# Optimization experiments

Measured on AMD Instinct MI355X. Metric: run time of the kernel, lower is better.

The kernel has to match this reference:

```python
import jax, jax.numpy as jnp
import numpy as np

B, N, D, A = 2048, 32, 64, 8
MAX_ACTION = 1.0
VARIANCE = 1.0


def setup_inputs() -> dict:
    key = jax.random.key(0)
    k1, k2, k3, k4, k5 = jax.random.split(key, 5)
    mean = jax.random.normal(k1, (B, D), dtype=jnp.float32)
    # SPD covariance: small-scale L L^T + 0.1 I
    L = jax.random.normal(k2, (B, D, D), dtype=jnp.float32) * 0.05
    covariance = jnp.einsum('bij,bkj->bik', L, L) + 0.1 * jnp.eye(D, dtype=jnp.float32)
    centers = jax.random.normal(k3, (N, D), dtype=jnp.float32) * 0.5
    weights = jax.random.normal(k4, (N, A), dtype=jnp.float32) * 0.1
    lengthscales = jnp.ones((D,), dtype=jnp.float32) + 0.1 * jax.random.uniform(k5, (D,), dtype=jnp.float32)
    return {"mean": mean, "covariance": covariance, "centers": centers,
            "weights": weights, "lengthscales": lengthscales}


def squash_sin(mean, covariance, max_action):
    # mean: (B, K); covariance: (B, K, K)
    K = mean.shape[-1]
    ma = jnp.full((K,), max_action, dtype=mean.dtype)
    diag_cov = jnp.diagonal(covariance, axis1=-2, axis2=-1)          # (B, K)
    squashed_mean = ma * jnp.exp(-diag_cov / 2.0) * jnp.sin(mean)
    lq = -(diag_cov[..., :, None] + diag_cov[..., None, :]) / 2.0
    q = jnp.exp(lq)
    mean_diff = mean[..., :, None] - mean[..., None, :]
    mean_sum = mean[..., :, None] + mean[..., None, :]
    sq_cov = ((jnp.exp(lq + covariance) - q) * jnp.cos(mean_diff)
              - (jnp.exp(lq - covariance) - q) * jnp.cos(mean_sum))
    outer_max = ma[None, :] * ma[:, None]
    sq_cov = outer_max * sq_cov / 2.0
    # diag_embed of (B, K) -> (B, K, K)
    cross = (ma * jnp.exp(-diag_cov / 2.0) * jnp.cos(mean))[..., :, None] * jnp.eye(K, dtype=mean.dtype)
    return squashed_mean, sq_cov, cross


def reference(mean, covariance, centers, weights, lengthscales):
    b = mean.shape[0]
    inv_l = 1.0 / lengthscales                                        # (D,)
    # B_mat = diag(inv_l) @ cov @ diag(inv_l) + I  (B, D, D)
    B_mat = covariance * (inv_l[:, None] * inv_l[None, :]) + jnp.eye(D, dtype=mean.dtype)
    inp = centers[None, :, :] - mean[:, None, :]                      # (B, N, D)
    scaled_inp = inp * inv_l                                          # (B, N, D)
    t = jnp.swapaxes(jnp.linalg.solve(B_mat, jnp.swapaxes(scaled_inp, -1, -2)), -1, -2)  # (B, N, D)
    exp_term = jnp.exp(-0.5 * jnp.sum(scaled_inp * t, axis=-1))       # (B, N)
    _, log_det = jnp.linalg.slogdet(B_mat)                            # (B,)
    normalizer = VARIANCE * jnp.exp(-0.5 * log_det)
    phi_mean = normalizer[:, None] * exp_term                         # (B, N)
    action_mean = phi_mean @ weights                                  # (B, A)

    t_scaled = t * inv_l                                              # (B, N, D)
    cross_cov = jnp.einsum('bnd,bna->bda', t_scaled, phi_mean[..., None] * weights)  # (B, D, A)

    diff = centers[:, None, :] - centers[None, :, :]                  # (N, N, D)
    center_bar = (centers[:, None, :] + centers[None, :, :]) / 2.0    # (N, N, D)
    inv_lambda = 1.0 / lengthscales ** 2
    exp1 = -0.25 * jnp.sum(diff ** 2 * inv_lambda, axis=-1)           # (N, N)
    B_q = covariance + jnp.diag(lengthscales ** 2 / 2.0)[None]        # (B, D, D)
    z = center_bar[None] - mean[:, None, None, :]                     # (B, N, N, D)
    z_flat = z.reshape(b, N * N, D)
    solved = jnp.swapaxes(jnp.linalg.solve(B_q, jnp.swapaxes(z_flat, -1, -2)), -1, -2)
    exp2 = (-0.5 * jnp.sum(z_flat * solved, axis=-1)).reshape(b, N, N)
    log_det_lh = jnp.sum(jnp.log(lengthscales ** 2 / 2.0))
    _, log_det_bq = jnp.linalg.slogdet(B_q)
    c_q = jnp.exp(0.5 * (log_det_lh - log_det_bq))                    # (B,)
    Q = (VARIANCE ** 2) * c_q[:, None, None] * jnp.exp(exp1[None] + exp2)  # (B, N, N)

    action_cov = jnp.einsum('na,bnm,mc->bac', weights, Q, weights)    # (B, A, A)
    action_cov = action_cov - action_mean[:, :, None] * action_mean[:, None, :]
    action_cov = (action_cov + jnp.swapaxes(action_cov, -1, -2)) / 2.0
    action_cov = action_cov + jnp.eye(A, dtype=mean.dtype) * 1e-6

    action_mean, action_cov, C = squash_sin(action_mean, action_cov, MAX_ACTION)
    cross_cov = jnp.einsum('bda,bac->bdc', cross_cov, C)
    return (action_mean, action_cov, cross_cov)
```

## Files before the change

kernel.cpp:

```cpp
#include <hip/hip_runtime.h>
#include <math.h>


#define DD 64
#define NN 32
#define AA 8
#define NBATCH 2048
#define STR 68
#define W9 9

__global__ void rbf_prep(const float* __restrict__ centers,
                         const float* __restrict__ ls,
                         float* __restrict__ ws) {
    __shared__ float cen_s[NN * DD];
    __shared__ float il2_s[DD];
    int t = threadIdx.x;
    for (int e = t; e < NN * DD; e += 256) cen_s[e] = centers[e];
    if (t < DD) { float l = ls[t]; il2_s[t] = 1.0f / (l * l); }
    __syncthreads();
    int p = blockIdx.x * 256 + t;
    if (p < NN * NN) {
        int n = p >> 5, m = p & 31;
        float acc = 0.f;
        for (int d = 0; d < DD; ++d) {
            float df = cen_s[n * DD + d] - cen_s[m * DD + d];
            acc += df * df * il2_s[d];
        }
        ws[p] = -0.25f * acc;
    }
    if (blockIdx.x == 0 && t < DD) {
        float l = ls[t];
        float v = logf(0.5f * l * l);
        #pragma unroll
        for (int o = 1; o < 64; o <<= 1) v += __shfl_xor(v, o, 64);
        if (t == 0) ws[NN * NN] = v;
    }
}

__device__ __forceinline__ void factor_panel(float (&A)[4][4], const int p,
    float* __restrict__ LmT, float* __restrict__ diag_s, float* __restrict__ invd_s,
    const int lw)
{
    const int rb  = lw & 15;
    const int cbl = lw >> 4;
    const int c0  = 16 * p + 4 * cbl;
    const int r0  = 4 * rb;
    #pragma unroll
    for (int jj = 0; jj < 16; ++jj) {
        const int q  = jj >> 2;
        const int ci = jj & 3;
        const int j  = 16 * p + jj;
        const int fsrc = rb | (q << 4);
        const int hsrc = (4 * p + cbl) | (q << 4);
        const int dsrc = (4 * p + q) | (q << 4);
        float d  = __shfl(A[ci][ci], dsrc, 64);
        float f0 = __shfl(A[0][ci], fsrc, 64);
        float f1 = __shfl(A[1][ci], fsrc, 64);
        float f2 = __shfl(A[2][ci], fsrc, 64);
        float f3 = __shfl(A[3][ci], fsrc, 64);
        float h0 = __shfl(A[0][ci], hsrc, 64);
        float h1 = __shfl(A[1][ci], hsrc, 64);
        float h2 = __shfl(A[2][ci], hsrc, 64);
        float h3 = __shfl(A[3][ci], hsrc, 64);
        float id = __builtin_amdgcn_rcpf(d);
        float fr[4];
        fr[0] = (r0 + 0 > j) ? f0 : 0.f;
        fr[1] = (r0 + 1 > j) ? f1 : 0.f;
        fr[2] = (r0 + 2 > j) ? f2 : 0.f;
        fr[3] = (r0 + 3 > j) ? f3 : 0.f;
        float hc[4];
        hc[0] = (c0 + 0 > j) ? h0 * id : 0.f;
        hc[1] = (c0 + 1 > j) ? h1 * id : 0.f;
        hc[2] = (c0 + 2 > j) ? h2 * id : 0.f;
        hc[3] = (c0 + 3 > j) ? h3 * id : 0.f;
        #pragma unroll
        for (int s = 0; s < 4; ++s)
            #pragma unroll
            for (int c = 0; c < 4; ++c)
                A[s][c] -= fr[s] * hc[c];
        if (cbl == 0) {
            float4 v = make_float4(fr[0] * id, fr[1] * id, fr[2] * id, fr[3] * id);
            *(float4*)&LmT[j * STR + r0] = v;
        }
        if (lw == jj) { diag_s[j] = d; invd_s[j] = id; }
    }
}

__device__ __forceinline__ void trailing_update2(
    float (&A1)[4][4], float (&A2)[4][4], const int p,
    const float* __restrict__ LmT1, const float* __restrict__ LmT2,
    const float* __restrict__ diag1, const float* __restrict__ diag2,
    const int rb, const int cb, const int cb1)
{
    #pragma unroll 2
    for (int kk = 0; kk < 16; ++kk) {
        const int k = 16 * p + kk;
        const float4 Lr1 = *(const float4*)&LmT1[k * STR + 4 * rb];
        const float4 Lc1 = *(const float4*)&LmT1[k * STR + 4 * cb1];
        const float4 Lr2 = *(const float4*)&LmT2[k * STR + 4 * rb];
        const float4 Lc2 = *(const float4*)&LmT2[k * STR + 4 * cb];
        const float d1 = diag1[k], d2 = diag2[k];
        {
            const float h0 = Lc1.x * d1, h1 = Lc1.y * d1, h2 = Lc1.z * d1, h3 = Lc1.w * d1;
            A1[0][0] -= Lr1.x * h0; A1[0][1] -= Lr1.x * h1; A1[0][2] -= Lr1.x * h2; A1[0][3] -= Lr1.x * h3;
            A1[1][0] -= Lr1.y * h0; A1[1][1] -= Lr1.y * h1; A1[1][2] -= Lr1.y * h2; A1[1][3] -= Lr1.y * h3;
            A1[2][0] -= Lr1.z * h0; A1[2][1] -= Lr1.z * h1; A1[2][2] -= Lr1.z * h2; A1[2][3] -= Lr1.z * h3;
            A1[3][0] -= Lr1.w * h0; A1[3][1] -= Lr1.w * h1; A1[3][2] -= Lr1.w * h2; A1[3][3] -= Lr1.w * h3;
        }
        {
            const float h0 = Lc2.x * d2, h1 = Lc2.y * d2, h2 = Lc2.z * d2, h3 = Lc2.w * d2;
            A2[0][0] -= Lr2.x * h0; A2[0][1] -= Lr2.x * h1; A2[0][2] -= Lr2.x * h2; A2[0][3] -= Lr2.x * h3;
            A2[1][0] -= Lr2.y * h0; A2[1][1] -= Lr2.y * h1; A2[1][2] -= Lr2.y * h2; A2[1][3] -= Lr2.y * h3;
            A2[2][0] -= Lr2.z * h0; A2[2][1] -= Lr2.z * h1; A2[2][2] -= Lr2.z * h2; A2[2][3] -= Lr2.z * h3;
            A2[3][0] -= Lr2.w * h0; A2[3][1] -= Lr2.w * h1; A2[3][2] -= Lr2.w * h2; A2[3][3] -= Lr2.w * h3;
        }
    }
}

__global__ __launch_bounds__(256, 3) void rbf_main(
    const float* __restrict__ mean,
    const float* __restrict__ cov,
    const float* __restrict__ centers,
    const float* __restrict__ weights,
    const float* __restrict__ ls,
    const float* __restrict__ ws,
    float* __restrict__ out)
{
    __shared__ __align__(16) float LmT1[DD * STR];
    __shared__ __align__(16) float LmT2[DD * STR];
    __shared__ __align__(16) float H_s[NN * STR];
    __shared__ __align__(16) float K_s[DD * W9];
    __shared__ __align__(16) float cp_s[DD * W9];
    __shared__ float diag1[DD], invd1[DD], diag2[DD], invd2[DD];
    __shared__ float mean_s[DD], invl_s[DD], l2h_s[DD];
    __shared__ float w9_s[NN * W9], phiw_s[NN * W9], U_s[NN * W9];
    __shared__ float am_s[AA], acr_s[AA * W9], Ca_s[AA];
    __shared__ float ldlh_s;

    const int t   = threadIdx.x;
    const int b   = blockIdx.x;
    const int lw  = t & 63;
    const int wv  = t >> 6;
    const int rb  = t & 15;
    const int cb  = t >> 4;
    const int cb1 = (cb + 8) & 15;
    const int grp = t >> 3;
    const int l8  = t & 7;
    const float* cvb = cov + (size_t)b * DD * DD;

    if (t < DD) {
        float l = ls[t];
        invl_s[t] = 1.0f / l;
        l2h_s[t]  = 0.5f * l * l;
        mean_s[t] = mean[(size_t)b * DD + t];
    }
    w9_s[(t >> 3) * W9 + (t & 7)] = weights[t];
    if (t == 0) ldlh_s = ws[NN * NN];
    __syncthreads();

    float A1[4][4], A2[4][4];
    {
        #pragma unroll
        for (int c = 0; c < 4; ++c) {
            const int gr = 4 * cb + c;
            const float4 cv = *(const float4*)(cvb + (size_t)gr * DD + 4 * rb);
            A2[0][c] = cv.x + ((4*rb+0 == gr) ? l2h_s[gr] : 0.0f);
            A2[1][c] = cv.y + ((4*rb+1 == gr) ? l2h_s[gr] : 0.0f);
            A2[2][c] = cv.z + ((4*rb+2 == gr) ? l2h_s[gr] : 0.0f);
            A2[3][c] = cv.w + ((4*rb+3 == gr) ? l2h_s[gr] : 0.0f);
        }
        const float il0 = invl_s[4*rb+0], il1 = invl_s[4*rb+1],
                    il2 = invl_s[4*rb+2], il3 = invl_s[4*rb+3];
        #pragma unroll
        for (int c = 0; c < 4; ++c) {
            const int gr = 4 * cb1 + c;
            const float4 cv = *(const float4*)(cvb + (size_t)gr * DD + 4 * rb);
            const float ilc = invl_s[gr];
            A1[0][c] = cv.x * il0 * ilc + ((4*rb+0 == gr) ? 1.0f : 0.0f);
            A1[1][c] = cv.y * il1 * ilc + ((4*rb+1 == gr) ? 1.0f : 0.0f);
            A1[2][c] = cv.z * il2 * ilc + ((4*rb+2 == gr) ? 1.0f : 0.0f);
            A1[3][c] = cv.w * il3 * ilc + ((4*rb+3 == gr) ? 1.0f : 0.0f);
        }
    }

    if (wv == 0) factor_panel(A2, 0, LmT2, diag2, invd2, lw);
    if (wv == 2) factor_panel(A1, 0, LmT1, diag1, invd1, lw);
    #pragma unroll 1
    for (int p = 0; p < 3; ++p) {
        __syncthreads();
        trailing_update2(A1, A2, p, LmT1, LmT2, diag1, diag2, rb, cb, cb1);
        if (wv == p + 1)         factor_panel(A2, p + 1, LmT2, diag2, invd2, lw);
        if (wv == ((p + 3) & 3)) factor_panel(A1, p + 1, LmT1, diag1, invd1, lw);
    }
    __syncthreads();

    float logdet1, cq;
    {
        float v1 = logf(diag1[lw]);
        float v2 = logf(diag2[lw]);
        #pragma unroll
        for (int o = 1; o < 64; o <<= 1) {
            v1 += __shfl_xor(v1, o, 64);
            v2 += __shfl_xor(v2, o, 64);
        }
        logdet1 = v1;
        cq = expf(0.5f * (ldlh_s - v2));
    }

    {
        float x1[8], x2[8];
        const float4 ca  = *(const float4*)(centers + grp * DD + 8 * l8);
        const float4 cb4 = *(const float4*)(centers + grp * DD + 8 * l8 + 4);
        {
            float d0 = ca.x  - mean_s[8*l8+0], d1 = ca.y  - mean_s[8*l8+1];
            float d2 = ca.z  - mean_s[8*l8+2], d3 = ca.w  - mean_s[8*l8+3];
            float d4 = cb4.x - mean_s[8*l8+4], d5 = cb4.y - mean_s[8*l8+5];
            float d6 = cb4.z - mean_s[8*l8+6], d7 = cb4.w - mean_s[8*l8+7];
            x1[0] = d0 * invl_s[8*l8+0]; x2[0] = 0.5f * d0;
            x1[1] = d1 * invl_s[8*l8+1]; x2[1] = 0.5f * d1;
            x1[2] = d2 * invl_s[8*l8+2]; x2[2] = 0.5f * d2;
            x1[3] = d3 * invl_s[8*l8+3]; x2[3] = 0.5f * d3;
            x1[4] = d4 * invl_s[8*l8+4]; x2[4] = 0.5f * d4;
            x1[5] = d5 * invl_s[8*l8+5]; x2[5] = 0.5f * d5;
            x1[6] = d6 * invl_s[8*l8+6]; x2[6] = 0.5f * d6;
            x1[7] = d7 * invl_s[8*l8+7]; x2[7] = 0.5f * d7;
        }
        for (int k8 = 0; k8 < 8; ++k8) {
            #pragma unroll
            for (int kk = 0; kk < 8; ++kk) {
                const int k = 8 * k8 + kk;
                const int src = (lw & 56) | k8;
                float z1 = __shfl(x1[kk], src, 64);
                float z2 = __shfl(x2[kk], src, 64);
                #pragma unroll
                for (int s = 0; s < 8; ++s) {
                    x1[s] -= LmT1[k * STR + 8 * l8 + s] * z1;
                    x2[s] -= LmT2[k * STR + 8 * l8 + s] * z2;
                }
            }
        }
        float qf = 0.f;
        #pragma unroll
        for (int s = 0; s < 8; ++s) qf += x1[s] * x1[s] * invd1[8 * l8 + s];
        qf += __shfl_xor(qf, 1, 64);
        qf += __shfl_xor(qf, 2, 64);
        qf += __shfl_xor(qf, 4, 64);
        float ph = expf(-0.5f * (logdet1 + qf));
        phiw_s[grp * W9 + l8] = ph * w9_s[grp * W9 + l8];
        #pragma unroll
        for (int s = 0; s < 8; ++s)
            H_s[grp * STR + 8 * l8 + s] = x2[s] * sqrtf(invd2[8 * l8 + s]);
    }
    __syncthreads();

    {
        float acc[4] = {0.f, 0.f, 0.f, 0.f};
        const int rot = 2 * l8;
        #pragma unroll 2
        for (int e = 0; e < 16; ++e) {
            const int e4 = 4 * ((e + rot) & 15);
            const float4 hn = *(const float4*)&H_s[grp * STR + e4];
            #pragma unroll
            for (int mm = 0; mm < 4; ++mm) {
                const float4 hm = *(const float4*)&H_s[(4 * l8 + mm) * STR + e4];
                float s0 = hn.x + hm.x, s1 = hn.y + hm.y;
                float s2 = hn.z + hm.z, s3 = hn.w + hm.w;
                acc[mm] += s0*s0 + s1*s1 + s2*s2 + s3*s3;
            }
        }
        const float4 e1 = *(const float4*)&ws[grp * NN + 4 * l8];
        float Q0 = cq * expf(e1.x - 0.5f * acc[0]);
        float Q1 = cq * expf(e1.y - 0.5f * acc[1]);
        float Q2 = cq * expf(e1.z - 0.5f * acc[2]);
        float Q3 = cq * expf(e1.w - 0.5f * acc[3]);
        float u[8];
        #pragma unroll
        for (int a = 0; a < 8; ++a) {
            u[a] = Q0 * w9_s[(4*l8+0)*W9 + a] + Q1 * w9_s[(4*l8+1)*W9 + a]
                 + Q2 * w9_s[(4*l8+2)*W9 + a] + Q3 * w9_s[(4*l8+3)*W9 + a];
            u[a] += __shfl_xor(u[a], 1, 64);
            u[a] += __shfl_xor(u[a], 2, 64);
            u[a] += __shfl_xor(u[a], 4, 64);
        }
        float uv = (l8 == 0) ? u[0] : (l8 == 1) ? u[1] : (l8 == 2) ? u[2] : (l8 == 3) ? u[3]
                 : (l8 == 4) ? u[4] : (l8 == 5) ? u[5] : (l8 == 6) ? u[6] : u[7];
        U_s[grp * W9 + l8] = uv;
    }
    {
        const int d = t >> 2, a0 = (t & 3) * 2;
        const float md = mean_s[d], il = invl_s[d];
        float k0 = 0.f, k1 = 0.f;
        for (int n = 0; n < NN; ++n) {
            float sv = (centers[n * DD + d] - md) * il;
            k0 += sv * phiw_s[n * W9 + a0];
            k1 += sv * phiw_s[n * W9 + a0 + 1];
        }
        K_s[d * W9 + a0]     = k0;
        K_s[d * W9 + a0 + 1] = k1;
    }
    __syncthreads();

    if (t < 64) {
        const int aa = t >> 3;
        float y[8];
        #pragma unroll
        for (int s = 0; s < 8; ++s) y[s] = K_s[(8 * l8 + s) * W9 + aa];
        for (int k8 = 0; k8 < 8; ++k8) {
            #pragma unroll
            for (int kk = 0; kk < 8; ++kk) {
                const int k = 8 * k8 + kk;
                float zk = __shfl(y[kk], (t & 56) | k8, 64);
                #pragma unroll
                for (int s = 0; s < 8; ++s)
                    y[s] -= LmT1[k * STR + 8 * l8 + s] * zk;
            }
        }
        #pragma unroll
        for (int s = 0; s < 8; ++s) y[s] *= invd1[8 * l8 + s];
        for (int i8 = 7; i8 >= 0; --i8) {
            #pragma unroll
            for (int ii = 7; ii >= 0; --ii) {
                const int i = 8 * i8 + ii;
                const float4 r0 = *(const float4*)&LmT1[i * STR + 8 * l8];
                const float4 r1 = *(const float4*)&LmT1[i * STR + 8 * l8 + 4];
                float part = r0.x*y[0] + r0.y*y[1] + r0.z*y[2] + r0.w*y[3]
                           + r1.x*y[4] + r1.y*y[5] + r1.z*y[6] + r1.w*y[7];
                part += __shfl_xor(part, 1, 64);
                part += __shfl_xor(part, 2, 64);
                part += __shfl_xor(part, 4, 64);
                if (l8 == i8) y[ii] -= part;
            }
        }
        #pragma unroll
        for (int s = 0; s < 8; ++s)
            cp_s[(8 * l8 + s) * W9 + aa] = y[s] * invl_s[8 * l8 + s];
    } else if (t < 72) {
        int a = t - 64;
        float am = 0.f;
        for (int n = 0; n < NN; ++n) am += phiw_s[n * W9 + a];
        am_s[a] = am;
    } else if (t >= 128 && t < 192) {
        int t2 = t - 128, a = t2 >> 3, c = t2 & 7;
        float acc2 = 0.f;
        for (int n = 0; n < NN; ++n) acc2 += w9_s[n * W9 + a] * U_s[n * W9 + c];
        acr_s[a * W9 + c] = acc2;
    }
    __syncthreads();

    float* out0 = out;
    float* out1 = out + (size_t)NBATCH * AA;
    float* out2 = out + (size_t)NBATCH * AA + (size_t)NBATCH * AA * AA;
    if (t < 64) {
        const int a = t >> 3, c = t & 7;
        const float ama = am_s[a], amc = am_s[c];
        const float vac = 0.5f * (acr_s[a * W9 + c] + acr_s[c * W9 + a])
                        - ama * amc + ((a == c) ? 1e-6f : 0.0f);
        const float dca = acr_s[a * W9 + a] - ama * ama + 1e-6f;
        const float dcc = acr_s[c * W9 + c] - amc * amc + 1e-6f;
        const float q = expf(-0.5f * (dca + dcc));
        const float sq = 0.5f * q * (expm1f(vac) * cosf(ama - amc)
                                   - expm1f(-vac) * cosf(ama + amc));
        out1[(size_t)b * 64 + t] = sq;
        if (t < AA) {
            float dct = acr_s[t * W9 + t] - am_s[t] * am_s[t] + 1e-6f;
            float e = expf(-0.5f * dct);
            out0[(size_t)b * AA + t] = e * sinf(am_s[t]);
            Ca_s[t] = e * cosf(am_s[t]);
        }
    }
    __syncthreads();
    #pragma unroll
    for (int e = 0; e < 2; ++e) {
        int idx = t + 256 * e;
        out2[(size_t)b * 512 + idx] = cp_s[(idx >> 3) * W9 + (idx & 7)] * Ca_s[idx & 7];
    }
}

extern "C" void kernel_launch(void* const* d_in, const int* in_sizes, int n_in,
                              void* d_out, int out_size, void* d_ws, size_t ws_size,
                              hipStream_t stream) {
    (void)in_sizes; (void)n_in; (void)out_size; (void)ws_size;
    const float* mean    = (const float*)d_in[0];
    const float* cov     = (const float*)d_in[1];
    const float* centers = (const float*)d_in[2];
    const float* weights = (const float*)d_in[3];
    const float* ls      = (const float*)d_in[4];
    float* ws = (float*)d_ws;
    float* o  = (float*)d_out;
    rbf_prep<<<4, 256, 0, stream>>>(centers, ls, ws);
    rbf_main<<<NBATCH, 256, 0, stream>>>(mean, cov, centers, weights, ls, ws, o);
}
```

Measured before the change: 231.2 us.

## Skip finished Cholesky tiles in trailing update and overlap Q computation with triangular solve

The trailing update is split per matrix, and each wave skips tiles whose columns are already factored. This avoids redundant FMAs and LDS reads in the blocked Cholesky. The Q/U computation now runs on waves 1-3 concurrently with the wave-0 triangular solve, instead of running on all threads beforehand. The K and am reductions are regrouped, at the cost of an extra barrier, a 24-group strided loop that leaves some imbalance, and possible divergence in the guarded trailing updates.

```diff
diff --git a/kernel.cpp b/kernel.cpp
--- a/kernel.cpp
+++ b/kernel.cpp
@@ -86,34 +86,21 @@
     }
 }
 
-__device__ __forceinline__ void trailing_update2(
-    float (&A1)[4][4], float (&A2)[4][4], const int p,
-    const float* __restrict__ LmT1, const float* __restrict__ LmT2,
-    const float* __restrict__ diag1, const float* __restrict__ diag2,
-    const int rb, const int cb, const int cb1)
+__device__ __forceinline__ void trailing_one(float (&A)[4][4], const int p,
+    const float* __restrict__ LmT, const float* __restrict__ diag_s,
+    const int rb, const int cbX)
 {
     #pragma unroll 2
     for (int kk = 0; kk < 16; ++kk) {
         const int k = 16 * p + kk;
-        const float4 Lr1 = *(const float4*)&LmT1[k * STR + 4 * rb];
-        const float4 Lc1 = *(const float4*)&LmT1[k * STR + 4 * cb1];
-        const float4 Lr2 = *(const float4*)&LmT2[k * STR + 4 * rb];
-        const float4 Lc2 = *(const float4*)&LmT2[k * STR + 4 * cb];
-        const float d1 = diag1[k], d2 = diag2[k];
-        {
-            const float h0 = Lc1.x * d1, h1 = Lc1.y * d1, h2 = Lc1.z * d1, h3 = Lc1.w * d1;
-            A1[0][0] -= Lr1.x * h0; A1[0][1] -= Lr1.x * h1; A1[0][2] -= Lr1.x * h2; A1[0][3] -= Lr1.x * h3;
-            A1[1][0] -= Lr1.y * h0; A1[1][1] -= Lr1.y * h1; A1[1][2] -= Lr1.y * h2; A1[1][3] -= Lr1.y * h3;
-            A1[2][0] -= Lr1.z * h0; A1[2][1] -= Lr1.z * h1; A1[2][2] -= Lr1.z * h2; A1[2][3] -= Lr1.z * h3;
-            A1[3][0] -= Lr1.w * h0; A1[3][1] -= Lr1.w * h1; A1[3][2] -= Lr1.w * h2; A1[3][3] -= Lr1.w * h3;
-        }
-        {
-            const float h0 = Lc2.x * d2, h1 = Lc2.y * d2, h2 = Lc2.z * d2, h3 = Lc2.w * d2;
-            A2[0][0] -= Lr2.x * h0; A2[0][1] -= Lr2.x * h1; A2[0][2] -= Lr2.x * h2; A2[0][3] -= Lr2.x * h3;
-            A2[1][0] -= Lr2.y * h0; A2[1][1] -= Lr2.y * h1; A2[1][2] -= Lr2.y * h2; A2[1][3] -= Lr2.y * h3;
-            A2[2][0] -= Lr2.z * h0; A2[2][1] -= Lr2.z * h1; A2[2][2] -= Lr2.z * h2; A2[2][3] -= Lr2.z * h3;
-            A2[3][0] -= Lr2.w * h0; A2[3][1] -= Lr2.w * h1; A2[3][2] -= Lr2.w * h2; A2[3][3] -= Lr2.w * h3;
-        }
+        const float4 Lr = *(const float4*)&LmT[k * STR + 4 * rb];
+        const float4 Lc = *(const float4*)&LmT[k * STR + 4 * cbX];
+        const float dk = diag_s[k];
+        const float h0 = Lc.x * dk, h1 = Lc.y * dk, h2 = Lc.z * dk, h3 = Lc.w * dk;
+        A[0][0] -= Lr.x * h0; A[0][1] -= Lr.x * h1; A[0][2] -= Lr.x * h2; A[0][3] -= Lr.x * h3;
+        A[1][0] -= Lr.y * h0; A[1][1] -= Lr.y * h1; A[1][2] -= Lr.y * h2; A[1][3] -= Lr.y * h3;
+        A[2][0] -= Lr.z * h0; A[2][1] -= Lr.z * h1; A[2][2] -= Lr.z * h2; A[2][3] -= Lr.z * h3;
+        A[3][0] -= Lr.w * h0; A[3][1] -= Lr.w * h1; A[3][2] -= Lr.w * h2; A[3][3] -= Lr.w * h3;
     }
 }
 
@@ -144,6 +131,7 @@
     const int rb  = t & 15;
     const int cb  = t >> 4;
     const int cb1 = (cb + 8) & 15;
+    const int wp1 = (wv + 2) & 3;
     const int grp = t >> 3;
     const int l8  = t & 7;
     const float* cvb = cov + (size_t)b * DD * DD;
@@ -188,7 +176,8 @@
     #pragma unroll 1
     for (int p = 0; p < 3; ++p) {
         __syncthreads();
-        trailing_update2(A1, A2, p, LmT1, LmT2, diag1, diag2, rb, cb, cb1);
+        if (wv  >= p + 1) trailing_one(A2, p, LmT2, diag2, rb, cb);
+        if (wp1 >= p + 1) trailing_one(A1, p, LmT1, diag1, rb, cb1);
         if (wv == p + 1)         factor_panel(A2, p + 1, LmT2, diag2, invd2, lw);
         if (wv == ((p + 3) & 3)) factor_panel(A1, p + 1, LmT1, diag1, invd1, lw);
     }
@@ -253,54 +242,30 @@
     }
     __syncthreads();
 
-    {
-        float acc[4] = {0.f, 0.f, 0.f, 0.f};
-        const int rot = 2 * l8;
-        #pragma unroll 2
-        for (int e = 0; e < 16; ++e) {
-            const int e4 = 4 * ((e + rot) & 15);
-            const float4 hn = *(const float4*)&H_s[grp * STR + e4];
-            #pragma unroll
-            for (int mm = 0; mm < 4; ++mm) {
-                const float4 hm = *(const float4*)&H_s[(4 * l8 + mm) * STR + e4];
-                float s0 = hn.x + hm.x, s1 = hn.y + hm.y;
-                float s2 = hn.z + hm.z, s3 = hn.w + hm.w;
-                acc[mm] += s0*s0 + s1*s1 + s2*s2 + s3*s3;
-            }
-        }
-        const float4 e1 = *(const float4*)&ws[grp * NN + 4 * l8];
-        float Q0 = cq * expf(e1.x - 0.5f * acc[0]);
-        float Q1 = cq * expf(e1.y - 0.5f * acc[1]);
-        float Q2 = cq * expf(e1.z - 0.5f * acc[2]);
-        float Q3 = cq * expf(e1.w - 0.5f * acc[3]);
-        float u[8];
-        #pragma unroll
-        for (int a = 0; a < 8; ++a) {
-            u[a] = Q0 * w9_s[(4*l8+0)*W9 + a] + Q1 * w9_s[(4*l8+1)*W9 + a]
-                 + Q2 * w9_s[(4*l8+2)*W9 + a] + Q3 * w9_s[(4*l8+3)*W9 + a];
-            u[a] += __shfl_xor(u[a], 1, 64);
-            u[a] += __shfl_xor(u[a], 2, 64);
-            u[a] += __shfl_xor(u[a], 4, 64);
-        }
-        float uv = (l8 == 0) ? u[0] : (l8 == 1) ? u[1] : (l8 == 2) ? u[2] : (l8 == 3) ? u[3]
-                 : (l8 == 4) ? u[4] : (l8 == 5) ? u[5] : (l8 == 6) ? u[6] : u[7];
-        U_s[grp * W9 + l8] = uv;
-    }
-    {
-        const int d = t >> 2, a0 = (t & 3) * 2;
+    if (t < 128) {
+        const int d = t >> 1, a0 = (t & 1) * 4;
         const float md = mean_s[d], il = invl_s[d];
-        float k0 = 0.f, k1 = 0.f;
+        float k0 = 0.f, k1 = 0.f, k2 = 0.f, k3 = 0.f;
         for (int n = 0; n < NN; ++n) {
             float sv = (centers[n * DD + d] - md) * il;
             k0 += sv * phiw_s[n * W9 + a0];
             k1 += sv * phiw_s[n * W9 + a0 + 1];
+            k2 += sv * phiw_s[n * W9 + a0 + 2];
+            k3 += sv * phiw_s[n * W9 + a0 + 3];
         }
         K_s[d * W9 + a0]     = k0;
         K_s[d * W9 + a0 + 1] = k1;
-    }
-    __syncthreads();
-
-    if (t < 64) {
+        K_s[d * W9 + a0 + 2] = k2;
+        K_s[d * W9 + a0 + 3] = k3;
+    } else if (t < 136) {
+        int a = t - 128;
+        float am = 0.f;
+        for (int n = 0; n < NN; ++n) am += phiw_s[n * W9 + a];
+        am_s[a] = am;
+    }
+    __syncthreads();
+
+    if (wv == 0) {
         const int aa = t >> 3;
         float y[8];
         #pragma unroll
@@ -334,13 +299,46 @@
         #pragma unroll
         for (int s = 0; s < 8; ++s)
             cp_s[(8 * l8 + s) * W9 + aa] = y[s] * invl_s[8 * l8 + s];
-    } else if (t < 72) {
-        int a = t - 64;
-        float am = 0.f;
-        for (int n = 0; n < NN; ++n) am += phiw_s[n * W9 + a];
-        am_s[a] = am;
-    } else if (t >= 128 && t < 192) {
-        int t2 = t - 128, a = t2 >> 3, c = t2 & 7;
+    } else {
+        const int g = (t - 64) >> 3;
+        for (int n = g; n < NN; n += 24) {
+            float acc[4] = {0.f, 0.f, 0.f, 0.f};
+            const int rot = 2 * l8;
+            #pragma unroll 2
+            for (int e = 0; e < 16; ++e) {
+                const int e4 = 4 * ((e + rot) & 15);
+                const float4 hn = *(const float4*)&H_s[n * STR + e4];
+                #pragma unroll
+                for (int mm = 0; mm < 4; ++mm) {
+                    const float4 hm = *(const float4*)&H_s[(4 * l8 + mm) * STR + e4];
+                    float s0 = hn.x + hm.x, s1 = hn.y + hm.y;
+                    float s2 = hn.z + hm.z, s3 = hn.w + hm.w;
+                    acc[mm] += s0*s0 + s1*s1 + s2*s2 + s3*s3;
+                }
+            }
+            const float4 e1 = *(const float4*)&ws[n * NN + 4 * l8];
+            float Q0 = cq * expf(e1.x - 0.5f * acc[0]);
+            float Q1 = cq * expf(e1.y - 0.5f * acc[1]);
+            float Q2 = cq * expf(e1.z - 0.5f * acc[2]);
+            float Q3 = cq * expf(e1.w - 0.5f * acc[3]);
+            float u[8];
+            #pragma unroll
+            for (int a = 0; a < 8; ++a) {
+                u[a] = Q0 * w9_s[(4*l8+0)*W9 + a] + Q1 * w9_s[(4*l8+1)*W9 + a]
+                     + Q2 * w9_s[(4*l8+2)*W9 + a] + Q3 * w9_s[(4*l8+3)*W9 + a];
+                u[a] += __shfl_xor(u[a], 1, 64);
+                u[a] += __shfl_xor(u[a], 2, 64);
+                u[a] += __shfl_xor(u[a], 4, 64);
+            }
+            float uv = (l8 == 0) ? u[0] : (l8 == 1) ? u[1] : (l8 == 2) ? u[2] : (l8 == 3) ? u[3]
+                     : (l8 == 4) ? u[4] : (l8 == 5) ? u[5] : (l8 == 6) ? u[6] : u[7];
+            U_s[n * W9 + l8] = uv;
+        }
+    }
+    __syncthreads();
+
+    if (t < 64) {
+        const int a = t >> 3, c = t & 7;
         float acc2 = 0.f;
         for (int n = 0; n < NN; ++n) acc2 += w9_s[n * W9 + a] * U_s[n * W9 + c];
         acr_s[a * W9 + c] = acc2;
```

Result: faster. 218.4 us (-5.5%).
